# Performance work log

Measured on AMD Instinct MI355X. Metric: run time of the kernel, lower is better.

## Reference

```python
import jax, jax.numpy as jnp
import numpy as np

H, D = 8, 8            # heads, per-head dim (hid_dim = 64)
HID = H * D
L = 6                  # HGTConv layers
NI, NV = 32768, 131072 # num 'instr' / 'var' nodes (batch_size == NI)
E_VV, E_VI, E_IV = 1048576, 524288, 524288
INV_SQRT_D = float(1.0 / np.sqrt(D))


def _seg_softmax(logits, seg, n):
    # softmax over edges grouped by destination node (PyG softmax semantics)
    m = jax.ops.segment_max(logits, seg, num_segments=n)
    m = jnp.where(jnp.isfinite(m), m, 0.0)
    e = jnp.exp(logits - m[seg])
    s = jax.ops.segment_sum(e, seg, num_segments=n)
    return e / (s[seg] + 1e-16)


def _edge_msg(k_src, v_src, q_dst, arel, mrel, prel, src, dst, n_dst):
    # relation-specific transforms: [N_src,H,D] x [H,D,D] -> [N_src,H,D]
    k_rel = jnp.einsum('nhd,hde->nhe', k_src, arel)
    v_rel = jnp.einsum('nhd,hde->nhe', v_src, mrel)
    alpha = jnp.einsum('ehd,ehd->eh', q_dst[dst], k_rel[src]) * prel * INV_SQRT_D  # [E,H]
    w = _seg_softmax(alpha, dst, n_dst)
    return jax.ops.segment_sum(v_rel[src] * w[:, :, None], dst, num_segments=n_dst)


def _kqv(x, Wk, Wq, Wv, bk, bq, bv, n):
    k = (x @ Wk.T + bk).reshape(n, H, D)
    q = (x @ Wq.T + bq).reshape(n, H, D)
    v = (x @ Wv.T + bv).reshape(n, H, D)
    return k, q, v


def _forward(x_instr, x_var,
             Wk_i, Wq_i, Wv_i, Wa_i, bk_i, bq_i, bv_i, ba_i, skip_i,
             Wk_v, Wq_v, Wv_v, Wa_v, bk_v, bq_v, bv_v, ba_v, skip_v,
             arel_vv, mrel_vv, prel_vv, arel_vi, mrel_vi, prel_vi,
             arel_iv, mrel_iv, prel_iv,
             Wqkv, bqkv, Wo, bo,
             mw0, mb0, mw1, mb1, mw2, mb2, mw3, mb3, mw4, mb4, mw5, mb5,
             src_vv, dst_vv, src_vi, dst_vi, src_iv, dst_iv):
    xi, xv = x_instr, x_var
    outs = []
    for l in range(L):
        k_i, q_i, v_i = _kqv(xi, Wk_i[l], Wq_i[l], Wv_i[l], bk_i[l], bq_i[l], bv_i[l], NI)
        k_v, q_v, v_v = _kqv(xv, Wk_v[l], Wq_v[l], Wv_v[l], bk_v[l], bq_v[l], bv_v[l], NV)
        # per-edge-type attention softmax + scatter-sum, then sum over edge types (group='sum')
        agg_v = (_edge_msg(k_v, v_v, q_v, arel_vv[l], mrel_vv[l], prel_vv[l], src_vv, dst_vv, NV)
                 + _edge_msg(k_i, v_i, q_v, arel_iv[l], mrel_iv[l], prel_iv[l], src_iv, dst_iv, NV))
        agg_i = _edge_msg(k_v, v_v, q_i, arel_vi[l], mrel_vi[l], prel_vi[l], src_vi, dst_vi, NI)
        o_i = jax.nn.gelu(agg_i.reshape(NI, HID), approximate=False) @ Wa_i[l].T + ba_i[l]
        b_i = jax.nn.sigmoid(skip_i[l])
        xi = b_i * o_i + (1.0 - b_i) * xi
        o_v = jax.nn.gelu(agg_v.reshape(NV, HID), approximate=False) @ Wa_v[l].T + ba_v[l]
        b_v = jax.nn.sigmoid(skip_v[l])
        xv = b_v * o_v + (1.0 - b_v) * xv
        if l > 0:
            outs.append(xi)
    # jumping-knowledge MultiheadAttention over the L-1 stacked layer outputs
    x = jnp.stack(outs)                        # [S, NI, HID], S = L-1 = 5
    S = x.shape[0]
    qkv = x @ Wqkv.T + bqkv                    # [S, NI, 3*HID]
    q, k, v = jnp.split(qkv, 3, axis=-1)
    q = q.reshape(S, NI, H, D)
    k = k.reshape(S, NI, H, D)
    v = v.reshape(S, NI, H, D)
    sc = jnp.einsum('snhd,tnhd->nhst', q, k) * INV_SQRT_D
    w = jax.nn.softmax(sc, axis=-1)
    o = jnp.einsum('nhst,tnhd->snhd', w, v).reshape(S, NI, HID)
    o = o @ Wo.T + bo
    out = o.sum(axis=0)                        # [NI, HID]; batch_size == NI so view is identity
    for W, b in ((mw0, mb0), (mw1, mb1), (mw2, mb2), (mw3, mb3), (mw4, mb4)):
        out = jax.nn.gelu(out @ W.T + b, approximate=False)
    out = out @ mw5.T + mb5                    # [NI, 1]
    return out[:, 0]


def setup_inputs() -> dict:
    key = jax.random.key(0)
    ks = iter(jax.random.split(key, 64))
    def nrm(shape, scale=1.0):
        return jax.random.normal(next(ks), shape, dtype=jnp.float32) * scale
    d = {}
    d['x_instr'] = nrm((NI, HID))
    d['x_var'] = nrm((NV, HID))
    for t in ('i', 'v'):
        for p in ('Wk', 'Wq', 'Wv', 'Wa'):
            d[f'{p}_{t}'] = nrm((L, HID, HID), (2.0 / HID) ** 0.5)
        for p in ('bk', 'bq', 'bv', 'ba'):
            d[f'{p}_{t}'] = jnp.zeros((L, HID), jnp.float32)
        d[f'skip_{t}'] = jnp.ones((L,), jnp.float32)
    for e in ('vv', 'vi', 'iv'):
        d[f'arel_{e}'] = nrm((L, H, D, D), (1.0 / D) ** 0.5)
        d[f'mrel_{e}'] = nrm((L, H, D, D), (1.0 / D) ** 0.5)
        d[f'prel_{e}'] = jnp.ones((L, H), jnp.float32)
    d['Wqkv'] = nrm((3 * HID, HID), (2.0 / HID) ** 0.5)
    d['bqkv'] = jnp.zeros((3 * HID,), jnp.float32)
    d['Wo'] = nrm((HID, HID), (2.0 / HID) ** 0.5)
    d['bo'] = jnp.zeros((HID,), jnp.float32)
    dims = [64, 32, 16, 8, 4, 2, 1]
    for i in range(6):
        d[f'mw{i}'] = nrm((dims[i + 1], dims[i]), (2.0 / dims[i]) ** 0.5)
        d[f'mb{i}'] = jnp.zeros((dims[i + 1],), jnp.float32)
    d['src_vv'] = jax.random.randint(next(ks), (E_VV,), 0, NV, dtype=jnp.int32).astype(jnp.int64)
    d['dst_vv'] = jax.random.randint(next(ks), (E_VV,), 0, NV, dtype=jnp.int32).astype(jnp.int64)
    d['src_vi'] = jax.random.randint(next(ks), (E_VI,), 0, NV, dtype=jnp.int32).astype(jnp.int64)
    d['dst_vi'] = jax.random.randint(next(ks), (E_VI,), 0, NI, dtype=jnp.int32).astype(jnp.int64)
    d['src_iv'] = jax.random.randint(next(ks), (E_IV,), 0, NI, dtype=jnp.int32).astype(jnp.int64)
    d['dst_iv'] = jax.random.randint(next(ks), (E_IV,), 0, NV, dtype=jnp.int32).astype(jnp.int64)
    return d


def reference(x_instr, x_var,
              Wk_i, Wq_i, Wv_i, Wa_i, bk_i, bq_i, bv_i, ba_i, skip_i,
              Wk_v, Wq_v, Wv_v, Wa_v, bk_v, bq_v, bv_v, ba_v, skip_v,
              arel_vv, mrel_vv, prel_vv, arel_vi, mrel_vi, prel_vi,
              arel_iv, mrel_iv, prel_iv,
              Wqkv, bqkv, Wo, bo,
              mw0, mb0, mw1, mb1, mw2, mb2, mw3, mb3, mw4, mb4, mw5, mb5,
              src_vv, dst_vv, src_vi, dst_vi, src_iv, dst_iv):
    return _forward(x_instr, x_var,
                    Wk_i, Wq_i, Wv_i, Wa_i, bk_i, bq_i, bv_i, ba_i, skip_i,
                    Wk_v, Wq_v, Wv_v, Wa_v, bk_v, bq_v, bv_v, ba_v, skip_v,
                    arel_vv, mrel_vv, prel_vv, arel_vi, mrel_vi, prel_vi,
                    arel_iv, mrel_iv, prel_iv,
                    Wqkv, bqkv, Wo, bo,
                    mw0, mb0, mw1, mb1, mw2, mb2, mw3, mb3, mw4, mb4, mw5, mb5,
                    src_vv, dst_vv, src_vi, dst_vi, src_iv, dst_iv)
```

## Files before the change

### kernel.cpp

```cpp
#include <hip/hip_runtime.h>
#include <cmath>

typedef _Float16 f16_t;
typedef __attribute__((ext_vector_type(8))) short short8;
typedef __attribute__((ext_vector_type(8))) _Float16 half8;
typedef __attribute__((ext_vector_type(4))) float f32x4;
typedef _Float16 h2v __attribute__((ext_vector_type(2)));
typedef _Float16 h8 __attribute__((ext_vector_type(8)));
typedef float f2 __attribute__((ext_vector_type(2)));

#define NI_N 32768
#define NV_N 131072
#define E_VV 1048576
#define E_VI 524288
#define E_IV 524288
#define NT_N (NV_N+NV_N+NI_N)
#define ET_N (E_VV+E_IV+E_VI)
#define SC_WIN 2
#define LOG2E 1.4426950408889634f
#define CHV 192
#define CHI 64
#define CHQ 256
#define EPAD 68

__device__ __forceinline__ float gelu_f(float x){ return 0.5f*x*(1.0f+erff(x*0.7071067811865476f)); }

__device__ __forceinline__ void splitf16(float v, short& hi, short& lo){
  f16_t h=(f16_t)v;
  hi=__builtin_bit_cast(short,h);
  f16_t l=(f16_t)(v-(float)h);
  lo=__builtin_bit_cast(short,l);
}
__device__ __forceinline__ f32x4 mfma16(short8 a, short8 b, f32x4 c){
  return __builtin_amdgcn_mfma_f32_16x16x32_f16(__builtin_bit_cast(half8,a),__builtin_bit_cast(half8,b),c,0,0,0);
}
__device__ __forceinline__ float fexp2(float x){
#if __has_builtin(__builtin_amdgcn_exp2f)
  return __builtin_amdgcn_exp2f(x);
#else
  return exp2f(x);
#endif
}
__device__ __forceinline__ float ldval(const float* p){ return *p; }
__device__ __forceinline__ float ldval(const f16_t* p){ return (float)*p; }
__device__ __forceinline__ void stval(float* p,float v){ *p=v; }
__device__ __forceinline__ void stval(f16_t* p,float v){ *p=(f16_t)v; }

__global__ __launch_bounds__(256) void k_hist3(const int* __restrict__ dvv,const int* __restrict__ div_,
    const int* __restrict__ dvi,int* __restrict__ cnt){
  int i=blockIdx.x*256+threadIdx.x;
  if(i<E_VV) atomicAdd(&cnt[dvv[i]],1);
  else if(i<E_VV+E_IV) atomicAdd(&cnt[NV_N+div_[i-E_VV]],1);
  else atomicAdd(&cnt[2*NV_N+dvi[i-E_VV-E_IV]],1);
}
__global__ __launch_bounds__(512) void k_scan1(const int* __restrict__ cnt,int N,int* __restrict__ rp,int* __restrict__ bsum){
  __shared__ int sh[512];
  int i=blockIdx.x*512+threadIdx.x;
  int v=(i<N)?cnt[i]:0;
  sh[threadIdx.x]=v; __syncthreads();
  for(int off=1;off<512;off<<=1){
    int t=(threadIdx.x>=(unsigned)off)?sh[threadIdx.x-off]:0; __syncthreads();
    sh[threadIdx.x]+=t; __syncthreads();
  }
  if(i<N) rp[i]=sh[threadIdx.x]-v;
  if(threadIdx.x==511) bsum[blockIdx.x]=sh[511];
}
__global__ __launch_bounds__(1024) void k_scan2(const int* __restrict__ bsum,int* __restrict__ boff,int nb){
  __shared__ int sh[1024];
  int t=threadIdx.x;
  int v=(t<nb)?bsum[t]:0;
  sh[t]=v; __syncthreads();
  for(int off=1;off<1024;off<<=1){
    int x=(t>=(unsigned)off)?sh[t-off]:0; __syncthreads();
    sh[t]+=x; __syncthreads();
  }
  if(t<nb) boff[t]=sh[t]-v;
  if(t==1023) boff[nb]=sh[1023];
}
__global__ __launch_bounds__(512) void k_scan3(int* __restrict__ rp,const int* __restrict__ boff,int* __restrict__ cur,int N,int nb){
  int i=blockIdx.x*512+threadIdx.x;
  if(i<N){ int v=rp[i]+boff[i>>9]; rp[i]=v; cur[i]=v; }
  if(i==0) rp[N]=boff[nb];
}
__global__ __launch_bounds__(256) void k_scatter3w(const int* __restrict__ svv,const int* __restrict__ dvv,
    const int* __restrict__ siv,const int* __restrict__ div_,
    const int* __restrict__ svi,const int* __restrict__ dvi,
    int* __restrict__ cur,int* __restrict__ esrc,int dlo,int dhi){
  int i=blockIdx.x*256+threadIdx.x;
  int d,s;
  if(i<E_VV){ d=dvv[i]; if(d<dlo||d>=dhi) return; s=svv[i]*320; }
  else if(i<E_VV+E_IV){ int j=i-E_VV; d=NV_N+div_[j]; if(d<dlo||d>=dhi) return; s=siv[j]*192; }
  else { int j=i-E_VV-E_IV; d=2*NV_N+dvi[j]; if(d<dlo||d>=dhi) return; s=svi[j]*320; }
  int p=atomicAdd(&cur[d],1); esrc[p]=s;
}

__global__ __launch_bounds__(256) void k_castx(const float* __restrict__ xi_in,const float* __restrict__ xv_in,
    f16_t* __restrict__ xi,f16_t* __restrict__ xv){
  int i=blockIdx.x*256+threadIdx.x;
  if(i<NI_N*64) xi[i]=(f16_t)xi_in[i];
  else { int j=i-NI_N*64; xv[j]=(f16_t)xv_in[j]; }
}

struct FoldArgs{
  const float *Wk_i,*Wq_i,*Wv_i,*bk_i,*bq_i,*bv_i;
  const float *Wk_v,*Wq_v,*Wv_v,*bk_v,*bq_v,*bv_v;
  const float *arel_vv,*mrel_vv,*prel_vv,*arel_vi,*mrel_vi,*prel_vi,*arel_iv,*mrel_iv,*prel_iv;
  const float *Wa_i,*Wa_v;
  short *fwh_var,*fwl_var,*fwh_ins,*fwl_ins,*wah_i,*wal_i,*wah_v,*wal_v;
  float *fwb_var,*fwb_ins;
};
__global__ __launch_bounds__(256) void k_fold6(FoldArgs fa){
  int gid=blockIdx.x*256+threadIdx.x;
  if(gid>=6*640*64) return;
  int l=gid/(640*64);
  int rem=gid-l*640*64;
  int r=rem>>6, c=rem&63;
  if(r>=512){
    int ro=r&63;
    const float* W=(r<576)?fa.Wa_i:fa.Wa_v;
    short *sh=((r<576)?fa.wah_i:fa.wah_v)+l*4096, *sl=((r<576)?fa.wal_i:fa.wal_v)+l*4096;
    short h,lo; splitf16(W[l*4096+ro*64+c],h,lo);
    sh[ro*64+c]=h; sl[ro*64+c]=lo;
    return;
  }
  const float *W,*B,*rel=nullptr,*prl=nullptr;
  short *sh,*sl; float *fwb; int orow; bool isq=false;
  if(r<320){
    sh=fa.fwh_var+l*320*64; sl=fa.fwl_var+l*320*64; fwb=fa.fwb_var+l*320; orow=r;
    if(r<64){ W=fa.Wq_v; B=fa.bq_v; isq=true; }
    else if(r<128){ W=fa.Wk_v; B=fa.bk_v; rel=fa.arel_vv; prl=fa.prel_vv; }
    else if(r<192){ W=fa.Wv_v; B=fa.bv_v; rel=fa.mrel_vv; }
    else if(r<256){ W=fa.Wk_v; B=fa.bk_v; rel=fa.arel_vi; prl=fa.prel_vi; }
    else         { W=fa.Wv_v; B=fa.bv_v; rel=fa.mrel_vi; }
  }else{
    int rr=r-320; sh=fa.fwh_ins+l*192*64; sl=fa.fwl_ins+l*192*64; fwb=fa.fwb_ins+l*192; orow=rr;
    if(rr<64){ W=fa.Wq_i; B=fa.bq_i; isq=true; }
    else if(rr<128){ W=fa.Wk_i; B=fa.bk_i; rel=fa.arel_iv; prl=fa.prel_iv; }
    else           { W=fa.Wv_i; B=fa.bv_i; rel=fa.mrel_iv; }
  }
  int d=orow&63;
  float val,bval;
  if(!rel){
    val=W[l*4096+d*64+c]; bval=B[l*64+d];
  }else{
    int h=d>>3, e=d&7;
    float s=prl?prl[l*8+h]*0.3535533905932738f:1.0f;
    float acc=0.f,bacc=0.f;
    #pragma unroll
    for(int dd=0;dd<8;dd++){
      float rv=rel[l*512+h*64+dd*8+e];
      acc += W[l*4096+(h*8+dd)*64+c]*rv;
      bacc+= B[l*64+h*8+dd]*rv;
    }
    val=acc*s; bval=bacc*s;
  }
  if(isq){ val*=LOG2E; bval*=LOG2E; }
  short h2q,lo2; splitf16(val,h2q,lo2);
  sh[orow*64+c]=h2q; sl[orow*64+c]=lo2;
  if(c==0) fwb[orow]=bval;
}

__global__ __launch_bounds__(256) void k_split2(const float* __restrict__ W,int n,short* __restrict__ hi,short* __restrict__ lo){
  int i=blockIdx.x*256+threadIdx.x;
  if(i<n){ short h,l2; splitf16(W[i],h,l2); hi[i]=h; lo[i]=l2; }
}

__device__ __forceinline__ void colres_body(const f16_t* __restrict__ A,int nrb,
    const short* __restrict__ Bh,const short* __restrict__ Bl,
    const float* __restrict__ bias,f16_t* __restrict__ out,int octot,int ocol0,
    int c,int CH,int wave,int lane,int m,int quad,f16_t (*rep)[72])
{
  short8 bhi[4][2], blo[4][2]; float bb[4];
  #pragma unroll
  for(int ot=0;ot<4;ot++){
    size_t o=(size_t)(ocol0+ot*16+m)*64+quad*8;
    bhi[ot][0]=*(const short8*)(Bh+o);    bhi[ot][1]=*(const short8*)(Bh+o+32);
    blo[ot][0]=*(const short8*)(Bl+o);    blo[ot][1]=*(const short8*)(Bl+o+32);
    bb[ot]=bias[ocol0+ot*16+m];
  }
  int rr0=lane>>3, seg=lane&7;
  for(int rb=c;rb<nrb;rb+=CH){
    int row0=rb*64+wave*16;
    const f16_t* ap=A+(size_t)(row0+m)*64+quad*8;
    short8 a0=*(const short8*)(const void*)ap;
    short8 a1=*(const short8*)(const void*)(ap+32);
    f32x4 acc[4];
    #pragma unroll
    for(int ot=0;ot<4;ot++){ f32x4 t={bb[ot],bb[ot],bb[ot],bb[ot]}; acc[ot]=t; }
    #pragma unroll
    for(int ot=0;ot<4;ot++){
      acc[ot]=mfma16(a0,blo[ot][0],acc[ot]);
      acc[ot]=mfma16(a0,bhi[ot][0],acc[ot]);
      acc[ot]=mfma16(a1,blo[ot][1],acc[ot]);
      acc[ot]=mfma16(a1,bhi[ot][1],acc[ot]);
    }
    #pragma unroll
    for(int ot=0;ot<4;ot++)
      #pragma unroll
      for(int r=0;r<4;r++)
        rep[quad*4+r][ot*16+m]=(f16_t)acc[ot][r];
    #pragma unroll
    for(int it=0;it<2;it++){
      int rr=it*8+rr0;
      h8 vals=*(const h8*)&rep[rr][seg*8];
      *(h8*)(out+(size_t)(row0+rr)*octot+ocol0+seg*8)=vals;
    }
  }
}

__global__ __launch_bounds__(256) void k_colres_feat(const f16_t* __restrict__ Av,const f16_t* __restrict__ Ai,
    const short* __restrict__ Bvh,const short* __restrict__ Bvl,const float* __restrict__ biasv,
    const short* __restrict__ Bih,const short* __restrict__ Bil,const float* __restrict__ biasi,
    f16_t* __restrict__ outv,f16_t* __restrict__ outi)
{
  __shared__ f16_t rep[4][16][72];
  const int wave=threadIdx.x>>6, lane=threadIdx.x&63;
  const int m=lane&15, quad=lane>>4;
  int bx=blockIdx.x;
  if(bx<5*CHV){
    int pan=bx/CHV, c=bx%CHV;
    colres_body(Av,NV_N/64,Bvh,Bvl,biasv,outv,320,pan*64,c,CHV,wave,lane,m,quad,rep[wave]);
  }else{
    bx-=5*CHV;
    int pan=bx/CHI, c=bx%CHI;
    colres_body(Ai,NI_N/64,Bih,Bil,biasi,outi,192,pan*64,c,CHI,wave,lane,m,quad,rep[wave]);
  }
}

__global__ __launch_bounds__(256) void k_colres1(const f16_t* __restrict__ A,int nrb,
    const short* __restrict__ Bh,const short* __restrict__ Bl,
    const float* __restrict__ bias,f16_t* __restrict__ out,int octot,int CH)
{
  __shared__ f16_t rep[4][16][72];
  const int wave=threadIdx.x>>6, lane=threadIdx.x&63;
  const int m=lane&15, quad=lane>>4;
  int pan=blockIdx.x/CH, c=blockIdx.x%CH;
  colres_body(A,nrb,Bh,Bl,bias,out,octot,pan*64,c,CH,wave,lane,m,quad,rep[wave]);
}

template<typename AT, typename OT>
__device__ __forceinline__ void gemm_body(const AT* __restrict__ A,int row0,
    const short* __restrict__ Bh,const short* __restrict__ Bl,
    const float* __restrict__ bias,float bias_scale,
    OT* __restrict__ out,int octot,int ocol0,int npanels,int m,int quad,int lane,
    f16_t (*rep)[72])
{
  const AT* ap=A+(size_t)(row0+m)*64+quad*8;
  constexpr bool AF16 = (sizeof(AT)==2);
  short8 ahi[2], alo[2];
  if constexpr(AF16){
    #pragma unroll
    for(int kf=0;kf<2;kf++) ahi[kf]=*(const short8*)(const void*)(ap+kf*32);
  }else{
    #pragma unroll
    for(int kf=0;kf<2;kf++){
      short8 th,tl;
      #pragma unroll
      for(int j=0;j<8;j++){ short h,l2; splitf16(ldval(&ap[kf*32+j]),h,l2); th[j]=h; tl[j]=l2; }
      ahi[kf]=th; alo[kf]=tl;
    }
  }
  for(int pan=0;pan<npanels;pan++){
    int colbase=pan*64;
    short8 bhi[4][2], blo[4][2];
    #pragma unroll
    for(int ot=0;ot<4;ot++){
      size_t o=(size_t)(colbase+ot*16+m)*64+quad*8;
      #pragma unroll
      for(int kf=0;kf<2;kf++){
        bhi[ot][kf]=*(const short8*)(Bh+o+kf*32);
        blo[ot][kf]=*(const short8*)(Bl+o+kf*32);
      }
    }
    f32x4 acc[4];
    #pragma unroll
    for(int ot=0;ot<4;ot++){
      float bv=bias[colbase+ot*16+m]*bias_scale;
      acc[ot][0]=bv; acc[ot][1]=bv; acc[ot][2]=bv; acc[ot][3]=bv;
    }
    #pragma unroll
    for(int ot=0;ot<4;ot++){
      #pragma unroll
      for(int kf=0;kf<2;kf++){
        if constexpr(!AF16) acc[ot]=mfma16(alo[kf],bhi[ot][kf],acc[ot]);
        acc[ot]=mfma16(ahi[kf],blo[ot][kf],acc[ot]);
        acc[ot]=mfma16(ahi[kf],bhi[ot][kf],acc[ot]);
      }
    }
    if constexpr(sizeof(OT)==2){
      #pragma unroll
      for(int ot=0;ot<4;ot++)
        #pragma unroll
        for(int r=0;r<4;r++)
          rep[quad*4+r][ot*16+m]=(f16_t)acc[ot][r];
      #pragma unroll
      for(int it=0;it<2;it++){
        int rr=it*8+(lane>>3), seg=lane&7;
        h8 vals=*(const h8*)&rep[rr][seg*8];
        *(h8*)(out+(size_t)(row0+rr)*octot+ocol0+colbase+seg*8)=vals;
      }
    }else{
      #pragma unroll
      for(int ot=0;ot<4;ot++){
        int col=ocol0+colbase+ot*16+m;
        #pragma unroll
        for(int r=0;r<4;r++){
          int row=row0+quad*4+r;
          stval(&out[(size_t)row*octot+col],acc[ot][r]);
        }
      }
    }
  }
}

template<typename AT, typename OT>
__global__ __launch_bounds__(256) void k_gemm64p(const AT* __restrict__ A,int N,
    const short* __restrict__ Bh,const short* __restrict__ Bl,
    const float* __restrict__ bias,float bias_scale,
    OT* __restrict__ out,int octot,int ocol0,int npanels)
{
  __shared__ f16_t rep[4][16][72];
  const int wave=threadIdx.x>>6, lane=threadIdx.x&63;
  const int m=lane&15, quad=lane>>4;
  const int row0=blockIdx.x*64+wave*16;
  if(row0>=N) return;
  gemm_body<AT,OT>(A,row0,Bh,Bl,bias,bias_scale,out,octot,ocol0,npanels,m,quad,lane,rep[wave]);
}

__global__ __launch_bounds__(256) void k_update2(const f16_t* __restrict__ agg_i,const f16_t* __restrict__ agg_v,
    const short* __restrict__ wah_i,const short* __restrict__ wal_i,
    const short* __restrict__ wah_v,const short* __restrict__ wal_v,
    const float* __restrict__ ba_i,const float* __restrict__ ba_v,
    const float* __restrict__ skip_i,const float* __restrict__ skip_v,
    f16_t* __restrict__ x_i,f16_t* __restrict__ x_v,
    f16_t* __restrict__ outs,int nbi)
{
  __shared__ f16_t rep[4][16][72];
  const int wave=threadIdx.x>>6, lane=threadIdx.x&63;
  const int m=lane&15, quad=lane>>4;
  const bool isI=(int)blockIdx.x<nbi;
  const int row0=(isI?blockIdx.x:(blockIdx.x-nbi))*64+wave*16;
  const f16_t* agg=isI?agg_i:agg_v;
  const short* Wah=isI?wah_i:wah_v;
  const short* Wal=isI?wal_i:wal_v;
  const float* ba=isI?ba_i:ba_v;
  const float* skip=isI?skip_i:skip_v;
  f16_t* x=isI?x_i:x_v;
  f16_t* oo=isI?outs:nullptr;
  f16_t (*R)[72]=rep[wave];
  short8 bhi[4][2], blo[4][2];
  #pragma unroll
  for(int ot=0;ot<4;ot++){
    size_t o=(size_t)(ot*16+m)*64+quad*8;
    #pragma unroll
    for(int kf=0;kf<2;kf++){
      bhi[ot][kf]=*(const short8*)(Wah+o+kf*32);
      blo[ot][kf]=*(const short8*)(Wal+o+kf*32);
    }
  }
  const f16_t* ap=agg+(size_t)(row0+m)*64+quad*8;
  short8 ahi[2], alo[2];
  #pragma unroll
  for(int kf=0;kf<2;kf++){
    short8 th,tl;
    #pragma unroll
    for(int j=0;j<8;j++){ short h,l2; splitf16(gelu_f((float)ap[kf*32+j]),h,l2); th[j]=h; tl[j]=l2; }
    ahi[kf]=th; alo[kf]=tl;
  }
  int rr0=lane>>3, seg=lane&7;
  h8 x0=*(const h8*)(x+(size_t)(row0+rr0)*64+seg*8);
  h8 x1=*(const h8*)(x+(size_t)(row0+8+rr0)*64+seg*8);
  *(h8*)&R[rr0][seg*8]=x0;
  *(h8*)&R[8+rr0][seg*8]=x1;
  f32x4 acc[4];
  #pragma unroll
  for(int ot=0;ot<4;ot++){
    float bv=ba[ot*16+m];
    acc[ot][0]=bv; acc[ot][1]=bv; acc[ot][2]=bv; acc[ot][3]=bv;
  }
  #pragma unroll
  for(int ot=0;ot<4;ot++){
    #pragma unroll
    for(int kf=0;kf<2;kf++){
      acc[ot]=mfma16(alo[kf],bhi[ot][kf],acc[ot]);
      acc[ot]=mfma16(ahi[kf],blo[ot][kf],acc[ot]);
      acc[ot]=mfma16(ahi[kf],bhi[ot][kf],acc[ot]);
    }
  }
  float s=1.0f/(1.0f+__expf(-skip[0]));
  #pragma unroll
  for(int ot=0;ot<4;ot++){
    int col=ot*16+m;
    #pragma unroll
    for(int r=0;r<4;r++){
      int row=quad*4+r;
      float xn=s*acc[ot][r]+(1.0f-s)*(float)R[row][col];
      R[row][col]=(f16_t)xn;
    }
  }
  h8 o0=*(const h8*)&R[rr0][seg*8];
  h8 o1=*(const h8*)&R[8+rr0][seg*8];
  *(h8*)(x+(size_t)(row0+rr0)*64+seg*8)=o0;
  *(h8*)(x+(size_t)(row0+8+rr0)*64+seg*8)=o1;
  if(oo){
    *(h8*)(oo+(size_t)(row0+rr0)*64+seg*8)=o0;
    *(h8*)(oo+(size_t)(row0+8+rr0)*64+seg*8)=o1;
  }
}

__device__ __forceinline__ float dot8(h8 k,h2v q0,h2v q1,h2v q2,h2v q3){
#if __has_builtin(__builtin_amdgcn_fdot2)
  float p=__builtin_amdgcn_fdot2((h2v){k[0],k[1]},q0,0.f,false);
  p=__builtin_amdgcn_fdot2((h2v){k[2],k[3]},q1,p,false);
  p=__builtin_amdgcn_fdot2((h2v){k[4],k[5]},q2,p,false);
  p=__builtin_amdgcn_fdot2((h2v){k[6],k[7]},q3,p,false);
  return p;
#else
  return (float)k[0]*(float)q0[0]+(float)k[1]*(float)q0[1]
        +(float)k[2]*(float)q1[0]+(float)k[3]*(float)q1[1]
        +(float)k[4]*(float)q2[0]+(float)k[5]*(float)q2[1]
        +(float)k[6]*(float)q3[0]+(float)k[7]*(float)q3[1];
#endif
}

__device__ __forceinline__ float edge_body(int b,int e,const int* __restrict__ es,
    const f16_t* __restrict__ sf,int koff,int e_slot,int lane,
    h2v q0,h2v q1,h2v q2,h2v q3,float* __restrict__ L,h8 pk,h8 pv)
{
  if(b>=e) return 0.f;
  float m=-1e30f, ls=0.f;
  f2 A0={0.f,0.f},A1={0.f,0.f},A2={0.f,0.f},A3={0.f,0.f};
  const int hb=(lane&7)*8;
  int off=0;
  if(b+8<e){ int ec=b+8+e_slot; ec=ec<e?ec:e-1; off=es[ec]; }
  {
    bool valid=(b+e_slot)<e;
    float p=dot8(pk,q0,q1,q2,q3);
    p=valid?p:-1e30f;
    float mn=fmaxf(m,p);
    float sc=fexp2(m-mn);
    float w=valid?fexp2(p-mn):0.f;
    ls=fmaf(ls,sc,w);
    f2 S={sc,sc},W={w,w};
    A0=A0*S+W*(f2){(float)pv[0],(float)pv[1]};
    A1=A1*S+W*(f2){(float)pv[2],(float)pv[3]};
    A2=A2*S+W*(f2){(float)pv[4],(float)pv[5]};
    A3=A3*S+W*(f2){(float)pv[6],(float)pv[7]};
    m=mn;
  }
  for(int i=b+8;i<e;i+=8){
    int inext=i+8;
    int offn=0;
    if(inext<e){ int ec=inext+e_slot; ec=ec<e?ec:e-1; offn=es[ec]; }
    const f16_t* kp=sf+(size_t)(unsigned)off+koff+hb;
    h8 kv=*(const h8*)kp;
    h8 vv=*(const h8*)(kp+64);
    bool valid=(i+e_slot)<e;
    float p=dot8(kv,q0,q1,q2,q3);
    p=valid?p:-1e30f;
    float mn=fmaxf(m,p);
    float sc=fexp2(m-mn);
    float w=valid?fexp2(p-mn):0.f;
    ls=fmaf(ls,sc,w);
    f2 S={sc,sc},W={w,w};
    A0=A0*S+W*(f2){(float)vv[0],(float)vv[1]};
    A1=A1*S+W*(f2){(float)vv[2],(float)vv[3]};
    A2=A2*S+W*(f2){(float)vv[4],(float)vv[5]};
    A3=A3*S+W*(f2){(float)vv[6],(float)vv[7]};
    m=mn;
    off=offn;
  }
  float mall=fmaxf(m,__shfl_xor(m,8));
  mall=fmaxf(mall,__shfl_xor(mall,16));
  mall=fmaxf(mall,__shfl_xor(mall,32));
  float scl=fexp2(m-mall);
  ls*=scl;
  float lsall=ls+__shfl_xor(ls,8);
  lsall+=__shfl_xor(lsall,16);
  lsall+=__shfl_xor(lsall,32);
  f2 S2={scl,scl};
  A0*=S2; A1*=S2; A2*=S2; A3*=S2;
  float* wp=L+e_slot*EPAD+hb;
  *(f32x4*)wp=(f32x4){A0[0],A0[1],A1[0],A1[1]};
  *(f32x4*)(wp+4)=(f32x4){A2[0],A2[1],A3[0],A3[1]};
  __asm__ volatile("s_waitcnt lgkmcnt(0)" ::: "memory");
  float r=0.f;
  #pragma unroll
  for(int ee=0;ee<8;ee++) r+=L[ee*EPAD+lane];
  float lsr=__shfl(lsall,lane>>3);
  return r/(lsr+1e-16f);
}

__global__ __launch_bounds__(256) void k_edge_all(const int* __restrict__ rp_all,const int* __restrict__ es,
    const f16_t* __restrict__ var_feat,const f16_t* __restrict__ ins_feat,
    f16_t* __restrict__ agg_v,f16_t* __restrict__ agg_i,int nbv)
{
  __shared__ float lds[4][8*EPAD];
  int wave=threadIdx.x>>6, lane=threadIdx.x&63;
  int e_slot=lane>>3, hb=(lane&7)*8;
  float* L=lds[wave];
  if((int)blockIdx.x<nbv){
    int n=blockIdx.x*4+wave;
    int b1=__builtin_amdgcn_readfirstlane(rp_all[n]);
    int e1=__builtin_amdgcn_readfirstlane(rp_all[n+1]);
    const int* rp2=rp_all+NV_N;
    int b2=__builtin_amdgcn_readfirstlane(rp2[n]);
    int e2=__builtin_amdgcn_readfirstlane(rp2[n+1]);
    h8 qv=*(const h8*)(var_feat+(size_t)n*320+hb);
    int off1=0,off2=0;
    if(b1<e1){ int ec=b1+e_slot; ec=ec<e1?ec:e1-1; off1=es[ec]; }
    if(b2<e2){ int ec=b2+e_slot; ec=ec<e2?ec:e2-1; off2=es[ec]; }
    h8 pk1={},pv1={},pk2={},pv2={};
    if(b1<e1){
      const f16_t* p1=var_feat+(size_t)(unsigned)off1+64+hb;
      pk1=*(const h8*)p1; pv1=*(const h8*)(p1+64);
    }
    if(b2<e2){
      const f16_t* p2=ins_feat+(size_t)(unsigned)off2+64+hb;
      pk2=*(const h8*)p2; pv2=*(const h8*)(p2+64);
    }
    h2v q0={qv[0],qv[1]},q1={qv[2],qv[3]},q2={qv[4],qv[5]},q3={qv[6],qv[7]};
    float r1=edge_body(b1,e1,es,var_feat,64,e_slot,lane,q0,q1,q2,q3,L,pk1,pv1);
    float r2=edge_body(b2,e2,es,ins_feat,64,e_slot,lane,q0,q1,q2,q3,L,pk2,pv2);
    agg_v[(size_t)n*64+lane]=(f16_t)(r1+r2);
  }else{
    int n=((int)blockIdx.x-nbv)*4+wave;
    const int* rp=rp_all+2*NV_N;
    int b=__builtin_amdgcn_readfirstlane(rp[n]);
    int e=__builtin_amdgcn_readfirstlane(rp[n+1]);
    h8 qv=*(const h8*)(ins_feat+(size_t)n*192+hb);
    int off0=0;
    if(b<e){ int ec=b+e_slot; ec=ec<e?ec:e-1; off0=es[ec]; }
    h8 pk={},pv={};
    if(b<e){
      const f16_t* p=var_feat+(size_t)(unsigned)off0+192+hb;
      pk=*(const h8*)p; pv=*(const h8*)(p+64);
    }
    h2v q0={qv[0],qv[1]},q1={qv[2],qv[3]},q2={qv[4],qv[5]},q3={qv[6],qv[7]};
    float r=edge_body(b,e,es,var_feat,192,e_slot,lane,q0,q1,q2,q3,L,pk,pv);
    agg_i[(size_t)n*64+lane]=(f16_t)r;
  }
}

__global__ __launch_bounds__(256) void k_jk(const f16_t* __restrict__ qkv,float* __restrict__ osum,int n_nodes){
  int wave=threadIdx.x>>6, lane=threadIdx.x&63;
  int n=blockIdx.x*4+wave;
  if(n>=n_nodes) return;
  float q[5],k[5],v[5];
  #pragma unroll
  for(int s=0;s<5;s++){
    const f16_t* p=qkv+((size_t)s*n_nodes+n)*192;
    q[s]=(float)p[lane]; k[s]=(float)p[64+lane]; v[s]=(float)p[128+lane];
  }
  float sc[5][5];
  #pragma unroll
  for(int s=0;s<5;s++)
    #pragma unroll
    for(int t=0;t<5;t++){
      float x=q[s]*k[t];
      x+=__shfl_xor(x,1); x+=__shfl_xor(x,2); x+=__shfl_xor(x,4);
      sc[s][t]=x*0.3535533905932738f;
    }
  float os=0.f;
  #pragma unroll
  for(int s=0;s<5;s++){
    float m=sc[s][0];
    #pragma unroll
    for(int t=1;t<5;t++) m=fmaxf(m,sc[s][t]);
    float den=0.f, acc=0.f;
    #pragma unroll
    for(int t=0;t<5;t++){ float e=__expf(sc[s][t]-m); den+=e; acc+=e*v[t]; }
    os+=acc/den;
  }
  osum[(size_t)n*64+lane]=os;
}

struct MlpArgs{ const float *w0,*b0,*w1,*b1,*w2,*b2,*w3,*b3,*w4,*b4,*w5,*b5; };
__global__ __launch_bounds__(256) void k_mlp(const float* __restrict__ in,MlpArgs ma,float* __restrict__ out,int N){
  __shared__ float sw0[2048],sb0[32],sw1[512],sb1[16],sw2[128],sb2[8],sw3[32],sb3[4],sw4[8],sb4[2],sw5[2],sb5[1];
  for(int i=threadIdx.x;i<2048;i+=256) sw0[i]=ma.w0[i];
  for(int i=threadIdx.x;i<512;i+=256)  sw1[i]=ma.w1[i];
  if(threadIdx.x<128) sw2[threadIdx.x]=ma.w2[threadIdx.x];
  if(threadIdx.x<32){ sb0[threadIdx.x]=ma.b0[threadIdx.x]; sw3[threadIdx.x]=ma.w3[threadIdx.x]; }
  if(threadIdx.x<16) sb1[threadIdx.x]=ma.b1[threadIdx.x];
  if(threadIdx.x<8){ sb2[threadIdx.x]=ma.b2[threadIdx.x]; sw4[threadIdx.x]=ma.w4[threadIdx.x]; }
  if(threadIdx.x<4) sb3[threadIdx.x]=ma.b3[threadIdx.x];
  if(threadIdx.x<2){ sb4[threadIdx.x]=ma.b4[threadIdx.x]; sw5[threadIdx.x]=ma.w5[threadIdx.x]; }
  if(threadIdx.x==0) sb5[0]=ma.b5[0];
  __syncthreads();
  int n=blockIdx.x*256+threadIdx.x;
  if(n>=N) return;
  float a[64];
  const f32x4* p4=(const f32x4*)(in+(size_t)n*64);
  #pragma unroll
  for(int j=0;j<16;j++){ f32x4 t=p4[j]; a[4*j]=t[0]; a[4*j+1]=t[1]; a[4*j+2]=t[2]; a[4*j+3]=t[3]; }
  float h1[32];
  #pragma unroll
  for(int o=0;o<32;o++){ float s=sb0[o];
    #pragma unroll
    for(int c=0;c<64;c++) s+=a[c]*sw0[o*64+c];
    h1[o]=gelu_f(s); }
  float h2q[16];
  #pragma unroll
  for(int o=0;o<16;o++){ float s=sb1[o];
    #pragma unroll
    for(int c=0;c<32;c++) s+=h1[c]*sw1[o*32+c];
    h2q[o]=gelu_f(s); }
  float h3[8];
  #pragma unroll
  for(int o=0;o<8;o++){ float s=sb2[o];
    #pragma unroll
    for(int c=0;c<16;c++) s+=h2q[c]*sw2[o*16+c];
    h3[o]=gelu_f(s); }
  float h4[4];
  #pragma unroll
  for(int o=0;o<4;o++){ float s=sb3[o];
    #pragma unroll
    for(int c=0;c<8;c++) s+=h3[c]*sw3[o*8+c];
    h4[o]=gelu_f(s); }
  float h5[2];
  #pragma unroll
  for(int o=0;o<2;o++){ float s=sb4[o];
    #pragma unroll
    for(int c=0;c<4;c++) s+=h4[c]*sw4[o*4+c];
    h5[o]=gelu_f(s); }
  float r=sb5[0]+h5[0]*sw5[0]+h5[1]*sw5[1];
  out[n]=r;
}

extern "C" void kernel_launch(void* const* d_in,const int* in_sizes,int n_in,
                              void* d_out,int out_size,void* d_ws,size_t ws_size,
                              hipStream_t stream){
  (void)in_sizes;(void)n_in;(void)out_size;(void)ws_size;
  const float* x_instr=(const float*)d_in[0];
  const float* x_var  =(const float*)d_in[1];
  const float* ba_i=(const float*)d_in[9];
  const float* skip_i=(const float*)d_in[10];
  const float* ba_v=(const float*)d_in[18];
  const float* skip_v=(const float*)d_in[19];
  const float* Wqkv=(const float*)d_in[29];
  const float* bqkv=(const float*)d_in[30];
  const float* Wo=(const float*)d_in[31];
  const float* bo=(const float*)d_in[32];
  const int* src_vv=(const int*)d_in[45];
  const int* dst_vv=(const int*)d_in[46];
  const int* src_vi=(const int*)d_in[47];
  const int* dst_vi=(const int*)d_in[48];
  const int* src_iv=(const int*)d_in[49];
  const int* dst_iv=(const int*)d_in[50];

  char* w=(char*)d_ws;
  auto alloc=[&](size_t b)->char*{ char* p=w; w+=(b+255)&~(size_t)255; return p; };
  int* rp_all=(int*)alloc((size_t)(NT_N+1)*4);
  int* cnt_all=(int*)alloc((size_t)NT_N*4);
  int* cur_all=(int*)alloc((size_t)NT_N*4);
  int* bsum =(int*)alloc(640*4);
  int* boff =(int*)alloc(640*4);
  int* esrc_all=(int*)alloc((size_t)ET_N*4);
  short* fwh_var=(short*)alloc((size_t)6*320*64*2);
  short* fwl_var=(short*)alloc((size_t)6*320*64*2);
  float* fwb_var=(float*)alloc((size_t)6*320*4);
  short* fwh_ins=(short*)alloc((size_t)6*192*64*2);
  short* fwl_ins=(short*)alloc((size_t)6*192*64*2);
  float* fwb_ins=(float*)alloc((size_t)6*192*4);
  short* wah_i=(short*)alloc((size_t)6*64*64*2);
  short* wal_i=(short*)alloc((size_t)6*64*64*2);
  short* wah_v=(short*)alloc((size_t)6*64*64*2);
  short* wal_v=(short*)alloc((size_t)6*64*64*2);
  short* qkvh=(short*)alloc(192*64*2);
  short* qkvl=(short*)alloc(192*64*2);
  short* woh=(short*)alloc(64*64*2);
  short* wol=(short*)alloc(64*64*2);
  f16_t* outs=(f16_t*)alloc((size_t)5*NI_N*64*2);
  char* arena=alloc((size_t)146800640);
  f16_t*  xv      =(f16_t*)(arena);
  f16_t*  xi      =(f16_t*)(arena+16777216);
  f16_t*  var_feat=(f16_t*)(arena+20971520);
  f16_t*  ins_feat=(f16_t*)(arena+104857600);
  f16_t*  agg_v   =(f16_t*)(arena+117440512);
  f16_t*  agg_i   =(f16_t*)(arena+134217728);
  f16_t*  qkv    =(f16_t*)(arena);
  float*  osum   =(float*)(arena+67108864);
  float*  out_jk =(float*)(arena+75497472);

  hipMemsetAsync(cnt_all,0,(size_t)NT_N*4,stream);
  k_hist3<<<ET_N/256,256,0,stream>>>(dst_vv,dst_iv,dst_vi,cnt_all);
  int nb=NT_N/512;
  k_scan1<<<nb,512,0,stream>>>(cnt_all,NT_N,rp_all,bsum);
  k_scan2<<<1,1024,0,stream>>>(bsum,boff,nb);
  k_scan3<<<nb,512,0,stream>>>(rp_all,boff,cur_all,NT_N,nb);
  for(int wdx=0;wdx<SC_WIN;wdx++){
    int dlo=wdx*(NT_N/SC_WIN), dhi=(wdx+1)*(NT_N/SC_WIN);
    k_scatter3w<<<ET_N/256,256,0,stream>>>(src_vv,dst_vv,src_iv,dst_iv,src_vi,dst_vi,cur_all,esrc_all,dlo,dhi);
  }

  k_castx<<<(NI_N*64+NV_N*64)/256,256,0,stream>>>(x_instr,x_var,xi,xv);

  k_split2<<<(192*64+255)/256,256,0,stream>>>(Wqkv,192*64,qkvh,qkvl);
  k_split2<<<(64*64+255)/256,256,0,stream>>>(Wo,64*64,woh,wol);

  FoldArgs fa;
  fa.Wk_i=(const float*)d_in[2]; fa.Wq_i=(const float*)d_in[3]; fa.Wv_i=(const float*)d_in[4];
  fa.bk_i=(const float*)d_in[6]; fa.bq_i=(const float*)d_in[7]; fa.bv_i=(const float*)d_in[8];
  fa.Wk_v=(const float*)d_in[11]; fa.Wq_v=(const float*)d_in[12]; fa.Wv_v=(const float*)d_in[13];
  fa.bk_v=(const float*)d_in[15]; fa.bq_v=(const float*)d_in[16]; fa.bv_v=(const float*)d_in[17];
  fa.arel_vv=(const float*)d_in[20]; fa.mrel_vv=(const float*)d_in[21]; fa.prel_vv=(const float*)d_in[22];
  fa.arel_vi=(const float*)d_in[23]; fa.mrel_vi=(const float*)d_in[24]; fa.prel_vi=(const float*)d_in[25];
  fa.arel_iv=(const float*)d_in[26]; fa.mrel_iv=(const float*)d_in[27]; fa.mrel_iv=(const float*)d_in[27]; fa.prel_iv=(const float*)d_in[28];
  fa.Wa_i=(const float*)d_in[5]; fa.Wa_v=(const float*)d_in[14];
  fa.fwh_var=fwh_var; fa.fwl_var=fwl_var; fa.fwh_ins=fwh_ins; fa.fwl_ins=fwl_ins;
  fa.wah_i=wah_i; fa.wal_i=wal_i; fa.wah_v=wah_v; fa.wal_v=wal_v;
  fa.fwb_var=fwb_var; fa.fwb_ins=fwb_ins;
  k_fold6<<<(6*640*64)/256,256,0,stream>>>(fa);

  for(int l=0;l<6;l++){
    k_colres_feat<<<5*CHV+3*CHI,256,0,stream>>>(xv,xi,
        fwh_var+(size_t)l*320*64,fwl_var+(size_t)l*320*64,fwb_var+l*320,
        fwh_ins+(size_t)l*192*64,fwl_ins+(size_t)l*192*64,fwb_ins+l*192,
        var_feat,ins_feat);
    k_edge_all<<<NV_N/4+NI_N/4,256,0,stream>>>(rp_all,esrc_all,var_feat,ins_feat,agg_v,agg_i,NV_N/4);
    k_update2<<<NI_N/64+NV_N/64,256,0,stream>>>(agg_i,agg_v,
        wah_i+(size_t)l*4096,wal_i+(size_t)l*4096,wah_v+(size_t)l*4096,wal_v+(size_t)l*4096,
        ba_i+l*64,ba_v+l*64,skip_i+l,skip_v+l,xi,xv,
        (l>0)?(outs+(size_t)(l-1)*NI_N*64):nullptr,NI_N/64);
  }

  k_colres1<<<3*CHQ,256,0,stream>>>(outs,5*NI_N/64,qkvh,qkvl,bqkv,qkv,192,CHQ);
  k_jk<<<NI_N/4,256,0,stream>>>(qkv,osum,NI_N);
  k_gemm64p<float,float><<<NI_N/64,256,0,stream>>>(osum,NI_N,woh,wol,bo,5.0f,out_jk,64,0,1);
  MlpArgs ma;
  ma.w0=(const float*)d_in[33]; ma.b0=(const float*)d_in[34];
  ma.w1=(const float*)d_in[35]; ma.b1=(const float*)d_in[36];
  ma.w2=(const float*)d_in[37]; ma.b2=(const float*)d_in[38];
  ma.w3=(const float*)d_in[39]; ma.b3=(const float*)d_in[40];
  ma.w4=(const float*)d_in[41]; ma.b4=(const float*)d_in[42];
  ma.w5=(const float*)d_in[43]; ma.b5=(const float*)d_in[44];
  k_mlp<<<NI_N/256,256,0,stream>>>(out_jk,ma,(float*)d_out,NI_N);
}
```

Baseline: 1.479 ms.

## Replace windowed CSR scatter with two-pass bucketed binning by destination

```diff
diff --git a/kernel.cpp b/kernel.cpp
--- a/kernel.cpp
+++ b/kernel.cpp
@@ -16,7 +16,7 @@
 #define E_IV 524288
 #define NT_N (NV_N+NV_N+NI_N)
 #define ET_N (E_VV+E_IV+E_VI)
-#define SC_WIN 2
+#define NBKT 576
 #define LOG2E 1.4426950408889634f
 #define CHV 192
 #define CHI 64
@@ -82,16 +82,28 @@
   if(i<N){ int v=rp[i]+boff[i>>9]; rp[i]=v; cur[i]=v; }
   if(i==0) rp[N]=boff[nb];
 }
-__global__ __launch_bounds__(256) void k_scatter3w(const int* __restrict__ svv,const int* __restrict__ dvv,
+__global__ __launch_bounds__(256) void k_binit(const int* __restrict__ rp,int* __restrict__ bcur){
+  int k=blockIdx.x*256+threadIdx.x;
+  if(k<NBKT) bcur[k]=rp[k<<9];
+}
+__global__ __launch_bounds__(256) void k_bin3(const int* __restrict__ svv,const int* __restrict__ dvv,
     const int* __restrict__ siv,const int* __restrict__ div_,
     const int* __restrict__ svi,const int* __restrict__ dvi,
-    int* __restrict__ cur,int* __restrict__ esrc,int dlo,int dhi){
+    int* __restrict__ bcur,int2* __restrict__ bpairs){
   int i=blockIdx.x*256+threadIdx.x;
   int d,s;
-  if(i<E_VV){ d=dvv[i]; if(d<dlo||d>=dhi) return; s=svv[i]*320; }
-  else if(i<E_VV+E_IV){ int j=i-E_VV; d=NV_N+div_[j]; if(d<dlo||d>=dhi) return; s=siv[j]*192; }
-  else { int j=i-E_VV-E_IV; d=2*NV_N+dvi[j]; if(d<dlo||d>=dhi) return; s=svi[j]*320; }
-  int p=atomicAdd(&cur[d],1); esrc[p]=s;
+  if(i<E_VV){ d=dvv[i]; s=svv[i]*320; }
+  else if(i<E_VV+E_IV){ int j=i-E_VV; d=NV_N+div_[j]; s=siv[j]*192; }
+  else { int j=i-E_VV-E_IV; d=2*NV_N+dvi[j]; s=svi[j]*320; }
+  int pos=atomicAdd(&bcur[d>>9],1);
+  bpairs[pos]=make_int2(d,s);
+}
+__global__ __launch_bounds__(256) void k_scatb(const int2* __restrict__ bpairs,
+    int* __restrict__ cur,int* __restrict__ esrc){
+  int i=blockIdx.x*256+threadIdx.x;
+  int2 pr=bpairs[i];
+  int p=atomicAdd(&cur[pr.x],1);
+  esrc[p]=pr.y;
 }
 
 __global__ __launch_bounds__(256) void k_castx(const float* __restrict__ xi_in,const float* __restrict__ xv_in,
@@ -656,6 +668,7 @@
   int* cur_all=(int*)alloc((size_t)NT_N*4);
   int* bsum =(int*)alloc(640*4);
   int* boff =(int*)alloc(640*4);
+  int* bcur =(int*)alloc(NBKT*4);
   int* esrc_all=(int*)alloc((size_t)ET_N*4);
   short* fwh_var=(short*)alloc((size_t)6*320*64*2);
   short* fwl_var=(short*)alloc((size_t)6*320*64*2);
@@ -679,6 +692,7 @@
   f16_t*  ins_feat=(f16_t*)(arena+104857600);
   f16_t*  agg_v   =(f16_t*)(arena+117440512);
   f16_t*  agg_i   =(f16_t*)(arena+134217728);
+  int2*   bpairs  =(int2*)(arena+20971520);
   f16_t*  qkv    =(f16_t*)(arena);
   float*  osum   =(float*)(arena+67108864);
   float*  out_jk =(float*)(arena+75497472);
@@ -689,10 +703,9 @@
   k_scan1<<<nb,512,0,stream>>>(cnt_all,NT_N,rp_all,bsum);
   k_scan2<<<1,1024,0,stream>>>(bsum,boff,nb);
   k_scan3<<<nb,512,0,stream>>>(rp_all,boff,cur_all,NT_N,nb);
-  for(int wdx=0;wdx<SC_WIN;wdx++){
-    int dlo=wdx*(NT_N/SC_WIN), dhi=(wdx+1)*(NT_N/SC_WIN);
-    k_scatter3w<<<ET_N/256,256,0,stream>>>(src_vv,dst_vv,src_iv,dst_iv,src_vi,dst_vi,cur_all,esrc_all,dlo,dhi);
-  }
+  k_binit<<<(NBKT+255)/256,256,0,stream>>>(rp_all,bcur);
+  k_bin3<<<ET_N/256,256,0,stream>>>(src_vv,dst_vv,src_iv,dst_iv,src_vi,dst_vi,bcur,bpairs);
+  k_scatb<<<ET_N/256,256,0,stream>>>(bpairs,cur_all,esrc_all);
 
   k_castx<<<(NI_N*64+NV_N*64)/256,256,0,stream>>>(x_instr,x_var,xi,xv);
 
@@ -706,7 +719,7 @@
   fa.bk_v=(const float*)d_in[15]; fa.bq_v=(const float*)d_in[16]; fa.bv_v=(const float*)d_in[17];
   fa.arel_vv=(const float*)d_in[20]; fa.mrel_vv=(const float*)d_in[21]; fa.prel_vv=(const float*)d_in[22];
   fa.arel_vi=(const float*)d_in[23]; fa.mrel_vi=(const float*)d_in[24]; fa.prel_vi=(const float*)d_in[25];
-  fa.arel_iv=(const float*)d_in[26]; fa.mrel_iv=(const float*)d_in[27]; fa.mrel_iv=(const float*)d_in[27]; fa.prel_iv=(const float*)d_in[28];
+  fa.arel_iv=(const float*)d_in[26]; fa.mrel_iv=(const float*)d_in[27]; fa.prel_iv=(const float*)d_in[28];
   fa.Wa_i=(const float*)d_in[5]; fa.Wa_v=(const float*)d_in[14];
   fa.fwh_var=fwh_var; fa.fwl_var=fwl_var; fa.fwh_ins=fwh_ins; fa.fwl_ins=fwl_ins;
   fa.wah_i=wah_i; fa.wal_i=wal_i; fa.wah_v=wah_v; fa.wal_v=wal_v;
```

Result: slower. 2.617 ms (+76.9%).
